# Kernel optimization log

Hardware: AMD Instinct MI355X
Metric: run time of the kernel (lower is better)

## Reference

```python
import jax, jax.numpy as jnp
import numpy as np

B, T, C = 4, 1024, 1024
H, D = 16, 64  # num_heads, head_channels
EPS = 1e-5


def layernorm(x, g, b):
    mu = jnp.mean(x, axis=-1, keepdims=True)
    d = x - mu
    var = jnp.mean(d * d, axis=-1, keepdims=True)
    return d * jax.lax.rsqrt(var + EPS) * g + b


def setup_inputs() -> dict:
    key = jax.random.key(0)
    ks = jax.random.split(key, 5)
    s = 0.02  # init scale for weights
    return {
        "x": jax.random.normal(ks[0], (B, T, C), jnp.float32),
        "norm_g": jnp.ones((C,), jnp.float32),
        "norm_b": jnp.zeros((C,), jnp.float32),
        "qkv_w": jax.random.normal(ks[1], (C, 3 * C), jnp.float32) * s,
        "qkv_b": jax.random.normal(ks[2], (3 * C,), jnp.float32) * s,
        "qln_g": jnp.ones((C,), jnp.float32),
        "qln_b": jnp.zeros((C,), jnp.float32),
        "kln_g": jnp.ones((C,), jnp.float32),
        "kln_b": jnp.zeros((C,), jnp.float32),
        "proj_w": jax.random.normal(ks[3], (C, C), jnp.float32) * s,
        "proj_b": jax.random.normal(ks[4], (C,), jnp.float32) * s,
    }


def reference(x, norm_g, norm_b, qkv_w, qkv_b, qln_g, qln_b, kln_g, kln_b, proj_w, proj_b):
    in_dtype = x.dtype
    # pre-LN computed in fp32, cast back to input dtype
    xn = layernorm(x.astype(jnp.float32), norm_g, norm_b).astype(in_dtype)
    qkv = xn @ qkv_w + qkv_b  # [B,T,3C]
    q, k, v = jnp.split(qkv, 3, axis=-1)
    # per-Q/K LayerNorm over the full channel dim (before head split)
    q = layernorm(q, qln_g, qln_b)
    k = layernorm(k, kln_g, kln_b)
    # [B,T,C] -> [B,H,T,D]
    to_heads = lambda t: t.reshape(B, T, H, D).transpose(0, 2, 1, 3)
    q, k, v = to_heads(q), to_heads(k), to_heads(v)
    temp = 1.0
    scale = (D ** -0.5) / temp  # sqrt_scale**2 / temp
    scores = jnp.einsum("bhqd,bhkd->bhqk", q, k) * scale
    attn = jax.nn.softmax(scores, axis=-1)
    out = jnp.einsum("bhqk,bhkd->bhqd", attn, v)
    out = out.transpose(0, 2, 1, 3).reshape(B, T, C)
    return out @ proj_w + proj_b
```

## Files before the change

kernel.cpp:

```cpp
#include <hip/hip_runtime.h>
#include <math.h>

#define T_SEQ 1024
#define C_DIM 1024
#define NB    4
#define NH    16
#define HD    64
#define C3    3072

typedef __attribute__((ext_vector_type(8))) short bf16x8;
typedef __attribute__((ext_vector_type(4))) float f32x4;
typedef unsigned short u16;

union B8 { bf16x8 v; u16 u[8]; unsigned d[4]; };

__device__ inline u16 bf16_rtn(float v) {
    unsigned int u = __float_as_uint(v);
    u += 0x7FFFu + ((u >> 16) & 1u);
    return (u16)(u >> 16);
}
__device__ inline void split_bf16(float v, u16& hi, u16& lo) {
    hi = bf16_rtn(v);
    float hif = __uint_as_float(((unsigned int)hi) << 16);
    lo = bf16_rtn(v - hif);
}

__global__ __launch_bounds__(256) void ln_split_kernel(const float* __restrict__ in,
                                                       u16* __restrict__ oh,
                                                       u16* __restrict__ ol,
                                                       const float* __restrict__ g,
                                                       const float* __restrict__ beta) {
    const int row = blockIdx.x;
    const float* x = in + (size_t)row * 1024;
    const int t = threadIdx.x;

    float4 v = *(const float4*)&x[t * 4];
    float s  = v.x + v.y + v.z + v.w;
    float ss = v.x * v.x + v.y * v.y + v.z * v.z + v.w * v.w;
    #pragma unroll
    for (int m = 1; m < 64; m <<= 1) {
        s  += __shfl_xor(s, m);
        ss += __shfl_xor(ss, m);
    }
    __shared__ float red[8];
    const int wave = t >> 6, lane = t & 63;
    if (lane == 0) { red[wave * 2] = s; red[wave * 2 + 1] = ss; }
    __syncthreads();
    s  = red[0] + red[2] + red[4] + red[6];
    ss = red[1] + red[3] + red[5] + red[7];

    const float mu   = s * (1.0f / 1024.0f);
    const float var  = ss * (1.0f / 1024.0f) - mu * mu;
    const float rstd = rsqrtf(var + 1e-5f);

    float4 gg = *(const float4*)&g[t * 4];
    float4 bb = *(const float4*)&beta[t * 4];
    float o[4];
    o[0] = (v.x - mu) * rstd * gg.x + bb.x;
    o[1] = (v.y - mu) * rstd * gg.y + bb.y;
    o[2] = (v.z - mu) * rstd * gg.z + bb.z;
    o[3] = (v.w - mu) * rstd * gg.w + bb.w;

    ushort4 h4, l4;
    split_bf16(o[0], h4.x, l4.x);
    split_bf16(o[1], h4.y, l4.y);
    split_bf16(o[2], h4.z, l4.z);
    split_bf16(o[3], h4.w, l4.w);
    size_t off = (size_t)row * 1024 + t * 4;
    *(ushort4*)&oh[off] = h4;
    *(ushort4*)&ol[off] = l4;
}

__global__ __launch_bounds__(256) void ln_qk_kernel(float* __restrict__ qkv,
                                                    const float* __restrict__ qg,
                                                    const float* __restrict__ qb,
                                                    const float* __restrict__ kg,
                                                    const float* __restrict__ kb,
                                                    u16* __restrict__ Kh,
                                                    u16* __restrict__ Kl) {
    const int row = blockIdx.x;
    const int isK = row >> 12;
    const int r = row & 4095;
    float* x = qkv + (size_t)r * C3 + (isK ? 1024 : 0);
    const float* g    = isK ? kg : qg;
    const float* beta = isK ? kb : qb;
    const int t = threadIdx.x;

    float4 v = *(const float4*)&x[t * 4];
    float s  = v.x + v.y + v.z + v.w;
    float ss = v.x * v.x + v.y * v.y + v.z * v.z + v.w * v.w;
    #pragma unroll
    for (int m = 1; m < 64; m <<= 1) {
        s  += __shfl_xor(s, m);
        ss += __shfl_xor(ss, m);
    }
    __shared__ float red[8];
    const int wave = t >> 6, lane = t & 63;
    if (lane == 0) { red[wave * 2] = s; red[wave * 2 + 1] = ss; }
    __syncthreads();
    s  = red[0] + red[2] + red[4] + red[6];
    ss = red[1] + red[3] + red[5] + red[7];

    const float mu   = s * (1.0f / 1024.0f);
    const float var  = ss * (1.0f / 1024.0f) - mu * mu;
    const float rstd = rsqrtf(var + 1e-5f);

    float4 gg = *(const float4*)&g[t * 4];
    float4 bb = *(const float4*)&beta[t * 4];
    float o0 = (v.x - mu) * rstd * gg.x + bb.x;
    float o1 = (v.y - mu) * rstd * gg.y + bb.y;
    float o2 = (v.z - mu) * rstd * gg.z + bb.z;
    float o3 = (v.w - mu) * rstd * gg.w + bb.w;

    if (!isK) {
        float4 o = {o0, o1, o2, o3};
        *(float4*)&x[t * 4] = o;
    } else {
        ushort4 h4, l4;
        split_bf16(o0, h4.x, l4.x);
        split_bf16(o1, h4.y, l4.y);
        split_bf16(o2, h4.z, l4.z);
        split_bf16(o3, h4.w, l4.w);
        const int c = t * 4;
        const int hh = c >> 6, d = c & 63;
        const int b = r >> 10, tt = r & 1023;
        size_t off = ((size_t)((b << 4) + hh) << 16) + (size_t)tt * 64 + d;
        *(ushort4*)&Kh[off] = h4;
        *(ushort4*)&Kl[off] = l4;
    }
}

__global__ __launch_bounds__(256) void vsplit_t(const float* __restrict__ qkv,
                                                u16* __restrict__ Vth,
                                                u16* __restrict__ Vtl) {
    __shared__ float tile[64][68];
    const int bid = blockIdx.x;
    const int tt = bid & 15, h = (bid >> 4) & 15, b = bid >> 8;
    const int t = threadIdx.x;
    const float* src = qkv + (size_t)(b * 1024 + tt * 64) * C3 + 2048 + h * 64;
    #pragma unroll
    for (int i = 0; i < 4; ++i) {
        int idx = i * 256 + t;
        int tr = idx >> 4, dc = (idx & 15) * 4;
        float4 v = *(const float4*)&src[(size_t)tr * C3 + dc];
        tile[tr][dc + 0] = v.x; tile[tr][dc + 1] = v.y;
        tile[tr][dc + 2] = v.z; tile[tr][dc + 3] = v.w;
    }
    __syncthreads();
    #pragma unroll
    for (int i = 0; i < 4; ++i) {
        int idx = i * 256 + t;
        int d = idx >> 4, tc = (idx & 15) * 4;
        ushort4 h4, l4;
        split_bf16(tile[tc + 0][d], h4.x, l4.x);
        split_bf16(tile[tc + 1][d], h4.y, l4.y);
        split_bf16(tile[tc + 2][d], h4.z, l4.z);
        split_bf16(tile[tc + 3][d], h4.w, l4.w);
        size_t off = ((size_t)((b * 16 + h) * 64 + d)) * 1024 + tt * 64 + tc;
        *(ushort4*)&Vth[off] = h4;
        *(ushort4*)&Vtl[off] = l4;
    }
}

__global__ __launch_bounds__(256) void wsplit_t(const float* __restrict__ W,
                                                u16* __restrict__ Th,
                                                u16* __restrict__ Tl,
                                                int K, int N, int ldt) {
    __shared__ float tile[64][69];
    const int n0 = blockIdx.x * 64, k0 = blockIdx.y * 64;
    const int t = threadIdx.x;
    #pragma unroll
    for (int i = 0; i < 4; ++i) {
        int idx = t + 256 * i;
        int kr = idx >> 4, nc = (idx & 15) * 4;
        float4 v = *(const float4*)&W[(size_t)(k0 + kr) * N + n0 + nc];
        tile[kr][nc + 0] = v.x; tile[kr][nc + 1] = v.y;
        tile[kr][nc + 2] = v.z; tile[kr][nc + 3] = v.w;
    }
    __syncthreads();
    #pragma unroll
    for (int i = 0; i < 4; ++i) {
        int idx = t + 256 * i;
        int nr = idx >> 4, kc = (idx & 15) * 4;
        ushort4 h4, l4;
        split_bf16(tile[kc + 0][nr], h4.x, l4.x);
        split_bf16(tile[kc + 1][nr], h4.y, l4.y);
        split_bf16(tile[kc + 2][nr], h4.z, l4.z);
        split_bf16(tile[kc + 3][nr], h4.w, l4.w);
        size_t o = (size_t)(n0 + nr) * ldt + k0 + kc;
        *(ushort4*)&Th[o] = h4;
        *(ushort4*)&Tl[o] = l4;
    }
}

__global__ __launch_bounds__(512, 2) void gemm256_mfma_split(
    const u16* __restrict__ Ah, const u16* __restrict__ Al,
    const u16* __restrict__ Bh, const u16* __restrict__ Bl,
    const float* __restrict__ bias, float* __restrict__ C,
    int N, int lda, int ldb) {
    __shared__ __align__(16) u16 SM[65536];

    const int t    = threadIdx.x;
    const int lane = t & 63;
    const int wid  = t >> 6;
    const int wr   = wid >> 2;
    const int wc   = wid & 3;
    const int m16  = lane & 15, g8 = lane >> 4;

    const int nbx = gridDim.x;
    const int nwg = nbx * gridDim.y;
    int bid = blockIdx.y * nbx + blockIdx.x;
    int swz = (bid & 7) * (nwg >> 3) + (bid >> 3);
    const int bn = (swz % nbx) * 256;
    const int bm = (swz / nbx) * 256;

    f32x4 acc[8][4];
    #pragma unroll
    for (int m = 0; m < 8; ++m)
        #pragma unroll
        for (int n = 0; n < 4; ++n) {
            f32x4 z = {0.0f, 0.0f, 0.0f, 0.0f};
            acc[m][n] = z;
        }

    auto STAGE = [&](int tile, int buf) {
        const int reg = tile >> 4;
        const u16* Ab = (reg == 1) ? Al : Ah;
        const u16* Bb = (reg == 2) ? Bl : Bh;
        const int kloc = (tile & 15) << 6;
        #pragma unroll
        for (int i = 0; i < 4; ++i) {
            const int idx = i * 512 + t;
            const int r = idx >> 3;
            const int cl = (idx & 7) ^ (r & 7);
            const size_t ga = ((size_t)(bm + r) * lda + kloc + cl * 8) * 2;
            const size_t gb = ((size_t)(bn + r) * ldb + kloc + cl * 8) * 2;
            const unsigned la = (unsigned)(buf * 32768 + idx * 16);
            const unsigned lb = (unsigned)(65536 + buf * 32768 + idx * 16);
            __builtin_amdgcn_global_load_lds(
                (const __attribute__((address_space(1))) void*)((const char*)Ab + ga),
                (__attribute__((address_space(3))) void*)((char*)SM + la), 16, 0, 0);
            __builtin_amdgcn_global_load_lds(
                (const __attribute__((address_space(1))) void*)((const char*)Bb + gb),
                (__attribute__((address_space(3))) void*)((char*)SM + lb), 16, 0, 0);
        }
    };

    STAGE(0, 0);
    STAGE(1, 1);
    asm volatile("s_waitcnt vmcnt(8)" ::: "memory");
    __builtin_amdgcn_s_barrier();
    __builtin_amdgcn_sched_barrier(0);

    for (int tt = 0; tt < 48; ++tt) {
        const int cb = tt & 1;
        const u16* Abuf = SM + cb * 16384;
        const u16* Bbuf = SM + 32768 + cb * 16384;

        bf16x8 bf[4][2];
        #pragma unroll
        for (int n = 0; n < 4; ++n)
            #pragma unroll
            for (int ks = 0; ks < 2; ++ks) {
                const int r = wc * 64 + n * 16 + m16;
                bf[n][ks] = *(const bf16x8*)&Bbuf[r * 64 + (((ks * 4 + g8) ^ (r & 7)) << 3)];
            }
        __builtin_amdgcn_s_setprio(1);
        #pragma unroll
        for (int m = 0; m < 8; ++m) {
            const int r = wr * 128 + m * 16 + m16;
            bf16x8 a0 = *(const bf16x8*)&Abuf[r * 64 + ((g8 ^ (r & 7)) << 3)];
            bf16x8 a1 = *(const bf16x8*)&Abuf[r * 64 + (((4 + g8) ^ (r & 7)) << 3)];
            #pragma unroll
            for (int n = 0; n < 4; ++n) {
                acc[m][n] = __builtin_amdgcn_mfma_f32_16x16x32_bf16(a0, bf[n][0], acc[m][n], 0, 0, 0);
                acc[m][n] = __builtin_amdgcn_mfma_f32_16x16x32_bf16(a1, bf[n][1], acc[m][n], 0, 0, 0);
            }
        }
        __builtin_amdgcn_s_setprio(0);

        __builtin_amdgcn_sched_barrier(0);
        __builtin_amdgcn_s_barrier();
        __builtin_amdgcn_sched_barrier(0);
        if (tt + 2 < 48) {
            STAGE(tt + 2, cb);
            __builtin_amdgcn_sched_barrier(0);
            asm volatile("s_waitcnt vmcnt(8)" ::: "memory");
        } else {
            asm volatile("s_waitcnt vmcnt(0)" ::: "memory");
        }
        __builtin_amdgcn_sched_barrier(0);
        __builtin_amdgcn_s_barrier();
        __builtin_amdgcn_sched_barrier(0);
    }

    #pragma unroll
    for (int m = 0; m < 8; ++m) {
        const int row0 = bm + wr * 128 + m * 16 + (g8 << 2);
        #pragma unroll
        for (int n = 0; n < 4; ++n) {
            const int col = bn + wc * 64 + n * 16 + m16;
            const float bv = bias[col];
            #pragma unroll
            for (int e = 0; e < 4; ++e)
                C[(size_t)(row0 + e) * N + col] = acc[m][n][e] + bv;
        }
    }
}

__global__ __launch_bounds__(256) void gemm_mfma_split(
    const u16* __restrict__ Ah, const u16* __restrict__ Al,
    const u16* __restrict__ Bh, const u16* __restrict__ Bl,
    const float* __restrict__ bias, float* __restrict__ C,
    int M, int N, int K, int lda, int ldb) {
    __shared__ u16 sAh[128 * 32], sAl[128 * 32], sBh[128 * 32], sBl[128 * 32];

    const int t    = threadIdx.x;
    const int lane = t & 63;
    const int wid  = t >> 6;
    const int wr   = wid >> 1, wc = wid & 1;

    const int nbx = gridDim.x;
    const int nwg = nbx * gridDim.y;
    int bid = blockIdx.y * nbx + blockIdx.x;
    int swz = (bid & 7) * (nwg >> 3) + (bid >> 3);
    const int bn = (swz % nbx) * 128;
    const int bm = (swz / nbx) * 128;

    const int jr    = lane >> 2;
    const int cphys = lane & 3;
    const int m16 = lane & 15, g8 = lane >> 4;

    f32x4 acc[4][4];
    #pragma unroll
    for (int m = 0; m < 4; ++m)
        #pragma unroll
        for (int n = 0; n < 4; ++n) {
            f32x4 z = {0.0f, 0.0f, 0.0f, 0.0f};
            acc[m][n] = z;
        }

    for (int k0 = 0; k0 < K; k0 += 32) {
        __syncthreads();
        #pragma unroll
        for (int jj = 0; jj < 2; ++jj) {
            const int j = wid * 2 + jj;
            const int r = (j << 4) + jr;
            const int cl = cphys ^ (r & 3);
            const size_t ga = ((size_t)(bm + r) * lda + k0 + (cl << 3)) * 2;
            const size_t gb = ((size_t)(bn + r) * ldb + k0 + (cl << 3)) * 2;
            const unsigned ldso = (unsigned)(j << 10);
            __builtin_amdgcn_global_load_lds(
                (const __attribute__((address_space(1))) void*)((const char*)Ah + ga),
                (__attribute__((address_space(3))) void*)((char*)sAh + ldso), 16, 0, 0);
            __builtin_amdgcn_global_load_lds(
                (const __attribute__((address_space(1))) void*)((const char*)Al + ga),
                (__attribute__((address_space(3))) void*)((char*)sAl + ldso), 16, 0, 0);
            __builtin_amdgcn_global_load_lds(
                (const __attribute__((address_space(1))) void*)((const char*)Bh + gb),
                (__attribute__((address_space(3))) void*)((char*)sBh + ldso), 16, 0, 0);
            __builtin_amdgcn_global_load_lds(
                (const __attribute__((address_space(1))) void*)((const char*)Bl + gb),
                (__attribute__((address_space(3))) void*)((char*)sBl + ldso), 16, 0, 0);
        }
        __syncthreads();

        bf16x8 ah[4], al[4], bh[4], bl[4];
        #pragma unroll
        for (int m = 0; m < 4; ++m) {
            const int r = wr * 64 + m * 16 + m16;
            const int off = (r << 5) + ((g8 ^ (m16 & 3)) << 3);
            ah[m] = *(const bf16x8*)&sAh[off];
            al[m] = *(const bf16x8*)&sAl[off];
        }
        #pragma unroll
        for (int n = 0; n < 4; ++n) {
            const int r = wc * 64 + n * 16 + m16;
            const int off = (r << 5) + ((g8 ^ (m16 & 3)) << 3);
            bh[n] = *(const bf16x8*)&sBh[off];
            bl[n] = *(const bf16x8*)&sBl[off];
        }
        #pragma unroll
        for (int m = 0; m < 4; ++m)
            #pragma unroll
            for (int n = 0; n < 4; ++n) {
                acc[m][n] = __builtin_amdgcn_mfma_f32_16x16x32_bf16(ah[m], bh[n], acc[m][n], 0, 0, 0);
                acc[m][n] = __builtin_amdgcn_mfma_f32_16x16x32_bf16(al[m], bh[n], acc[m][n], 0, 0, 0);
                acc[m][n] = __builtin_amdgcn_mfma_f32_16x16x32_bf16(ah[m], bl[n], acc[m][n], 0, 0, 0);
            }
    }

    #pragma unroll
    for (int m = 0; m < 4; ++m) {
        const int row0 = bm + wr * 64 + m * 16 + (g8 << 2);
        #pragma unroll
        for (int n = 0; n < 4; ++n) {
            const int col = bn + wc * 64 + n * 16 + m16;
            const float bv = bias[col];
            #pragma unroll
            for (int e = 0; e < 4; ++e)
                C[(size_t)(row0 + e) * N + col] = acc[m][n][e] + bv;
        }
    }
}

__global__ __launch_bounds__(256) void attn_mfma(const float* __restrict__ qkv,
                                                 const u16* __restrict__ Kh,
                                                 const u16* __restrict__ Kl,
                                                 const u16* __restrict__ Vth,
                                                 const u16* __restrict__ Vtl,
                                                 u16* __restrict__ att) {
    __shared__ __align__(16) u16 SM[32768];

    const int t    = threadIdx.x;
    const int lane = t & 63;
    const int wv   = t >> 6;
    const int m16  = lane & 15, g8 = lane >> 4;

    const int bid  = blockIdx.x;
    const int work = (bid & 7) * 128 + (bid >> 3);
    const int qt = work & 15;
    const int bh = work >> 4;
    const int h  = bh & 15;
    const int b  = bh >> 4;
    const int q0 = qt * 64;

    const int srow = lane >> 3;
    const int scl  = (lane & 7) ^ srow;
    const size_t kvrow0 = (size_t)bh << 16;

    auto stageK = [&](int kt) {
        const int kb = kt * 64;
        #pragma unroll
        for (int issue = 0; issue < 2; ++issue) {
            const int rloc = (issue * 4 + wv) * 8 + srow;
            const size_t go = (kvrow0 + (size_t)(kb + rloc) * 64 + scl * 8) * 2;
            const unsigned lo = (unsigned)((issue * 4 + wv) * 1024);
            __builtin_amdgcn_global_load_lds(
                (const __attribute__((address_space(1))) void*)((const char*)Kh + go),
                (__attribute__((address_space(3))) void*)((char*)SM + lo), 16, 0, 0);
            __builtin_amdgcn_global_load_lds(
                (const __attribute__((address_space(1))) void*)((const char*)Kl + go),
                (__attribute__((address_space(3))) void*)((char*)SM + 8192 + lo), 16, 0, 0);
        }
    };
    auto stageV = [&](int kt, int bsel) {
        const int kb = kt * 64;
        #pragma unroll
        for (int issue = 0; issue < 2; ++issue) {
            const int rloc = (issue * 4 + wv) * 8 + srow;
            const size_t go = (kvrow0 + (size_t)rloc * 1024 + kb + scl * 8) * 2;
            const unsigned lo = (unsigned)(16384 + bsel * 16384 + (issue * 4 + wv) * 1024);
            __builtin_amdgcn_global_load_lds(
                (const __attribute__((address_space(1))) void*)((const char*)Vth + go),
                (__attribute__((address_space(3))) void*)((char*)SM + lo), 16, 0, 0);
            __builtin_amdgcn_global_load_lds(
                (const __attribute__((address_space(1))) void*)((const char*)Vtl + go),
                (__attribute__((address_space(3))) void*)((char*)SM + 8192 + lo), 16, 0, 0);
        }
    };

    bf16x8 qh[2], ql[2];
    {
        const float* qrow = qkv + (size_t)(b * T_SEQ + q0 + wv * 16 + m16) * C3 + h * HD;
        #pragma unroll
        for (int ds = 0; ds < 2; ++ds) {
            float4 a = *(const float4*)&qrow[ds * 32 + g8 * 8];
            float4 c = *(const float4*)&qrow[ds * 32 + g8 * 8 + 4];
            float q8[8] = {a.x, a.y, a.z, a.w, c.x, c.y, c.z, c.w};
            B8 hh, ll;
            #pragma unroll
            for (int j = 0; j < 8; ++j) {
                u16 hi, lo;
                split_bf16(q8[j] * 0.125f, hi, lo);
                hh.u[j] = hi; ll.u[j] = lo;
            }
            qh[ds] = hh.v; ql[ds] = ll.v;
        }
    }

    f32x4 acc_o[4];
    #pragma unroll
    for (int i = 0; i < 4; ++i) { f32x4 z = {0, 0, 0, 0}; acc_o[i] = z; }
    float m_run = -INFINITY, l_run = 0.0f;

    u16* Phw = SM + 24576 + wv * 1024;
    u16* Plw = SM + 28672 + wv * 1024;

    stageK(0);
    stageV(0, 0);
    asm volatile("s_waitcnt vmcnt(0)" ::: "memory");
    __builtin_amdgcn_s_barrier();
    __builtin_amdgcn_sched_barrier(0);

    int vsel = 0;
    for (int kt = 0; kt < 16; ++kt) {
        f32x4 accs[4];
        #pragma unroll
        for (int i = 0; i < 4; ++i) { f32x4 z = {0, 0, 0, 0}; accs[i] = z; }
        #pragma unroll
        for (int ds = 0; ds < 2; ++ds) {
            #pragma unroll
            for (int sub = 0; sub < 4; ++sub) {
                const int row = sub * 16 + m16;
                const int idx = row * 64 + ((((ds * 4 + g8)) ^ (m16 & 7)) << 3);
                bf16x8 kh = *(const bf16x8*)&SM[idx];
                bf16x8 kl = *(const bf16x8*)&SM[4096 + idx];
                accs[sub] = __builtin_amdgcn_mfma_f32_16x16x32_bf16(kh, qh[ds], accs[sub], 0, 0, 0);
                accs[sub] = __builtin_amdgcn_mfma_f32_16x16x32_bf16(kl, qh[ds], accs[sub], 0, 0, 0);
                accs[sub] = __builtin_amdgcn_mfma_f32_16x16x32_bf16(kh, ql[ds], accs[sub], 0, 0, 0);
            }
        }

        __builtin_amdgcn_sched_barrier(0);
        __builtin_amdgcn_s_barrier();
        __builtin_amdgcn_sched_barrier(0);
        if (kt < 15) { stageK(kt + 1); stageV(kt + 1, vsel ^ 1); }

        float mt = accs[0][0];
        #pragma unroll
        for (int sub = 0; sub < 4; ++sub)
            #pragma unroll
            for (int e = 0; e < 4; ++e) mt = fmaxf(mt, accs[sub][e]);
        mt = fmaxf(mt, __shfl_xor(mt, 16));
        mt = fmaxf(mt, __shfl_xor(mt, 32));
        const float mnew = fmaxf(m_run, mt);
        const float fsc = __expf(m_run - mnew);
        float p[4][4];
        float ts = 0.0f;
        #pragma unroll
        for (int sub = 0; sub < 4; ++sub)
            #pragma unroll
            for (int e = 0; e < 4; ++e) {
                p[sub][e] = __expf(accs[sub][e] - mnew);
                ts += p[sub][e];
            }
        ts += __shfl_xor(ts, 16);
        ts += __shfl_xor(ts, 32);
        l_run = l_run * fsc + ts;
        m_run = mnew;
        #pragma unroll
        for (int d = 0; d < 4; ++d)
            #pragma unroll
            for (int e = 0; e < 4; ++e) acc_o[d][e] *= fsc;

        #pragma unroll
        for (int sub = 0; sub < 4; ++sub)
            #pragma unroll
            for (int pp = 0; pp < 2; ++pp) {
                float p0 = p[sub][2 * pp], p1 = p[sub][2 * pp + 1];
                u16 h0, l0, h1, l1;
                split_bf16(p0, h0, l0);
                split_bf16(p1, h1, l1);
                unsigned hw = (unsigned)h0 | ((unsigned)h1 << 16);
                unsigned lw = (unsigned)l0 | ((unsigned)l1 << 16);
                const int idx = m16 * 64 + (((2 * sub + (g8 >> 1)) ^ (m16 & 7)) << 3)
                                + 4 * (g8 & 1) + 2 * pp;
                *(unsigned*)&Phw[idx] = hw;
                *(unsigned*)&Plw[idx] = lw;
            }

        bf16x8 pfh[2], pfl[2];
        #pragma unroll
        for (int ks = 0; ks < 2; ++ks) {
            const int idx = m16 * 64 + ((((ks * 4 + g8)) ^ (m16 & 7)) << 3);
            pfh[ks] = *(const bf16x8*)&Phw[idx];
            pfl[ks] = *(const bf16x8*)&Plw[idx];
        }

        const int vb = 8192 + vsel * 8192;
        #pragma unroll
        for (int dsub = 0; dsub < 4; ++dsub) {
            #pragma unroll
            for (int ks = 0; ks < 2; ++ks) {
                const int vrow = dsub * 16 + m16;
                const int vidx = vb + vrow * 64 + ((((ks * 4 + g8)) ^ (m16 & 7)) << 3);
                bf16x8 vh = *(const bf16x8*)&SM[vidx];
                bf16x8 vl = *(const bf16x8*)&SM[4096 + vidx];
                acc_o[dsub] = __builtin_amdgcn_mfma_f32_16x16x32_bf16(vh, pfh[ks], acc_o[dsub], 0, 0, 0);
                acc_o[dsub] = __builtin_amdgcn_mfma_f32_16x16x32_bf16(vh, pfl[ks], acc_o[dsub], 0, 0, 0);
                acc_o[dsub] = __builtin_amdgcn_mfma_f32_16x16x32_bf16(vl, pfh[ks], acc_o[dsub], 0, 0, 0);
            }
        }

        __builtin_amdgcn_sched_barrier(0);
        asm volatile("s_waitcnt vmcnt(0)" ::: "memory");
        __builtin_amdgcn_s_barrier();
        __builtin_amdgcn_sched_barrier(0);
        vsel ^= 1;
    }

    const float linv = 1.0f / l_run;
    #pragma unroll
    for (int dsub = 0; dsub < 4; ++dsub)
        #pragma unroll
        for (int pp = 0; pp < 2; ++pp) {
            float o0 = acc_o[dsub][2 * pp] * linv;
            float o1 = acc_o[dsub][2 * pp + 1] * linv;
            u16 h0, l0, h1, l1;
            split_bf16(o0, h0, l0);
            split_bf16(o1, h1, l1);
            unsigned hw = (unsigned)h0 | ((unsigned)h1 << 16);
            unsigned lw = (unsigned)l0 | ((unsigned)l1 << 16);
            const int idx = m16 * 64 + (((2 * dsub + (g8 >> 1)) ^ (m16 & 7)) << 3)
                            + 4 * (g8 & 1) + 2 * pp;
            *(unsigned*)&Phw[idx] = hw;
            *(unsigned*)&Plw[idx] = lw;
        }
    __syncthreads();
    #pragma unroll
    for (int i = 0; i < 2; ++i) {
        int s = t + 256 * i;
        int q_l = s >> 3, dg8 = s & 7;
        const int idx = q_l * 64 + ((dg8 ^ (q_l & 7)) << 3);
        bf16x8 oh = *(const bf16x8*)&SM[24576 + idx];
        bf16x8 ol = *(const bf16x8*)&SM[28672 + idx];
        size_t off = (size_t)(b * T_SEQ + q0 + q_l) * 6144 + 2048 + h * HD + dg8 * 8;
        *(bf16x8*)&att[off] = oh;
        *(bf16x8*)&att[off + 1024] = ol;
    }
}

extern "C" void kernel_launch(void* const* d_in, const int* in_sizes, int n_in,
                              void* d_out, int out_size, void* d_ws, size_t ws_size,
                              hipStream_t stream) {
    const float* x      = (const float*)d_in[0];
    const float* norm_g = (const float*)d_in[1];
    const float* norm_b = (const float*)d_in[2];
    const float* qkv_w  = (const float*)d_in[3];
    const float* qkv_b  = (const float*)d_in[4];
    const float* qln_g  = (const float*)d_in[5];
    const float* qln_b  = (const float*)d_in[6];
    const float* kln_g  = (const float*)d_in[7];
    const float* kln_b  = (const float*)d_in[8];
    const float* proj_w = (const float*)d_in[9];
    const float* proj_b = (const float*)d_in[10];
    float* out = (float*)d_out;

    char* w = (char*)d_ws;
    float* qkv    = (float*)w;
    u16* qkv_u16  = (u16*)w;
    u16* xn_hi    = (u16*)(w + 50331648);
    u16* xn_lo    = (u16*)(w + 58720256);
    u16* wq_hi    = (u16*)(w + 67108864);
    u16* wq_lo    = (u16*)(w + 73400320);
    u16* Kh       = xn_hi;
    u16* Kl       = xn_lo;
    u16* Vth      = (u16*)(w + 67108864);
    u16* Vtl      = (u16*)(w + 75497472);
    u16* pw_hi    = qkv_u16 + 4096;
    u16* pw_lo    = qkv_u16 + 5120;
    u16* att_hi   = qkv_u16 + 2048;
    u16* att_lo   = qkv_u16 + 3072;

    const int rows = NB * T_SEQ;

    ln_split_kernel<<<rows, 256, 0, stream>>>(x, xn_hi, xn_lo, norm_g, norm_b);
    wsplit_t<<<dim3(C3 / 64, C_DIM / 64), 256, 0, stream>>>(qkv_w, wq_hi, wq_lo, C_DIM, C3, 1024);
    gemm256_mfma_split<<<dim3(C3 / 256, rows / 256), 512, 0, stream>>>(
        xn_hi, xn_lo, wq_hi, wq_lo, qkv_b, qkv, C3, 1024, 1024);
    ln_qk_kernel<<<2 * rows, 256, 0, stream>>>(qkv, qln_g, qln_b, kln_g, kln_b, Kh, Kl);
    vsplit_t<<<1024, 256, 0, stream>>>(qkv, Vth, Vtl);
    wsplit_t<<<dim3(C_DIM / 64, C_DIM / 64), 256, 0, stream>>>(proj_w, pw_hi, pw_lo, C_DIM, C_DIM, 6144);
    attn_mfma<<<1024, 256, 0, stream>>>(qkv, Kh, Kl, Vth, Vtl, qkv_u16);
    gemm_mfma_split<<<dim3(C_DIM / 128, rows / 128), 256, 0, stream>>>(
        att_hi, att_lo, pw_hi, pw_lo, proj_b, out, rows, C_DIM, C_DIM, 6144, 6144);
}
```

Measured before the change: 330.5 us.

## Restructure QKV GEMM mainloop into four-phase interleaved load/compute pipeline

Rewrites the 256x256 split-bf16 QKV GEMM main loop so each K-tile is split into two 32-wide halves stored in separate LDS regions. Global-to-LDS staging is issued in small per-wave chunks interleaved with four MFMA phases per iteration, with barriers between phases. The goal is to overlap memory traffic with MFMA work more finely and cut register pressure from the fragment loads. Launch bounds drop from 2 to 1 waves per SIMD, which allows more registers but may lower occupancy. The extra barriers and the more intricate vmcnt accounting add synchronization cost and room for ordering errors.

```diff
diff --git a/kernel.cpp b/kernel.cpp
--- a/kernel.cpp
+++ b/kernel.cpp
@@ -193,7 +193,7 @@
     }
 }
 
-__global__ __launch_bounds__(512, 2) void gemm256_mfma_split(
+__global__ __launch_bounds__(512, 1) void gemm256_8ph(
     const u16* __restrict__ Ah, const u16* __restrict__ Al,
     const u16* __restrict__ Bh, const u16* __restrict__ Bl,
     const float* __restrict__ bias, float* __restrict__ C,
@@ -223,71 +223,130 @@
             acc[m][n] = z;
         }
 
-    auto STAGE = [&](int tile, int buf) {
+    const int srow = lane >> 2;
+    const int scol = lane & 3;
+
+    auto STAGE1 = [&](int tile, int ks, int part, int buf) {
+        if (tile > 47) return;
         const int reg = tile >> 4;
-        const u16* Ab = (reg == 1) ? Al : Ah;
-        const u16* Bb = (reg == 2) ? Bl : Bh;
-        const int kloc = (tile & 15) << 6;
-        #pragma unroll
-        for (int i = 0; i < 4; ++i) {
-            const int idx = i * 512 + t;
-            const int r = idx >> 3;
-            const int cl = (idx & 7) ^ (r & 7);
-            const size_t ga = ((size_t)(bm + r) * lda + kloc + cl * 8) * 2;
-            const size_t gb = ((size_t)(bn + r) * ldb + kloc + cl * 8) * 2;
-            const unsigned la = (unsigned)(buf * 32768 + idx * 16);
-            const unsigned lb = (unsigned)(65536 + buf * 32768 + idx * 16);
-            __builtin_amdgcn_global_load_lds(
-                (const __attribute__((address_space(1))) void*)((const char*)Ab + ga),
-                (__attribute__((address_space(3))) void*)((char*)SM + la), 16, 0, 0);
-            __builtin_amdgcn_global_load_lds(
-                (const __attribute__((address_space(1))) void*)((const char*)Bb + gb),
-                (__attribute__((address_space(3))) void*)((char*)SM + lb), 16, 0, 0);
+        const u16* src = part == 0 ? ((reg == 1) ? Al : Ah)
+                                   : ((reg == 2) ? Bl : Bh);
+        const int ld = part == 0 ? lda : ldb;
+        const int r0 = part == 0 ? bm : bn;
+        const int kloc = ((tile & 15) << 6) + (ks << 5);
+        const unsigned mb = (unsigned)(part * 65536 + buf * 32768 + ks * 16384 + wid * 2048);
+        #pragma unroll
+        for (int j = 0; j < 2; ++j) {
+            const int row = wid * 32 + j * 16 + srow;
+            const int cl = scol ^ (row & 3);
+            const size_t ga = ((size_t)(r0 + row) * ld + kloc + cl * 8) * 2;
+            __builtin_amdgcn_global_load_lds(
+                (const __attribute__((address_space(1))) void*)((const char*)src + ga),
+                (__attribute__((address_space(3))) void*)((char*)SM + mb + j * 1024),
+                16, 0, 0);
         }
     };
 
-    STAGE(0, 0);
-    STAGE(1, 1);
+    STAGE1(0, 0, 0, 0); STAGE1(0, 0, 1, 0);
+    STAGE1(0, 1, 0, 0); STAGE1(0, 1, 1, 0);
+    STAGE1(1, 0, 0, 1); STAGE1(1, 0, 1, 1);
+    __builtin_amdgcn_sched_barrier(0);
     asm volatile("s_waitcnt vmcnt(8)" ::: "memory");
+    __builtin_amdgcn_sched_barrier(0);
     __builtin_amdgcn_s_barrier();
     __builtin_amdgcn_sched_barrier(0);
 
     for (int tt = 0; tt < 48; ++tt) {
         const int cb = tt & 1;
-        const u16* Abuf = SM + cb * 16384;
-        const u16* Bbuf = SM + 32768 + cb * 16384;
-
-        bf16x8 bf[4][2];
-        #pragma unroll
-        for (int n = 0; n < 4; ++n)
-            #pragma unroll
-            for (int ks = 0; ks < 2; ++ks) {
-                const int r = wc * 64 + n * 16 + m16;
-                bf[n][ks] = *(const bf16x8*)&Bbuf[r * 64 + (((ks * 4 + g8) ^ (r & 7)) << 3)];
-            }
+        const int aB = cb * 16384;
+        const int bB = 32768 + cb * 16384;
+        bf16x8 bfr[4], afr[4];
+
+        #pragma unroll
+        for (int n = 0; n < 4; ++n) {
+            const int r = wc * 64 + n * 16 + m16;
+            bfr[n] = *(const bf16x8*)&SM[bB + r * 32 + ((g8 ^ (r & 3)) << 3)];
+        }
+        #pragma unroll
+        for (int m = 0; m < 4; ++m) {
+            const int r = wr * 128 + m * 16 + m16;
+            afr[m] = *(const bf16x8*)&SM[aB + r * 32 + ((g8 ^ (r & 3)) << 3)];
+        }
+        STAGE1(tt + 1, 1, 0, cb ^ 1);
         __builtin_amdgcn_s_setprio(1);
         #pragma unroll
-        for (int m = 0; m < 8; ++m) {
-            const int r = wr * 128 + m * 16 + m16;
-            bf16x8 a0 = *(const bf16x8*)&Abuf[r * 64 + ((g8 ^ (r & 7)) << 3)];
-            bf16x8 a1 = *(const bf16x8*)&Abuf[r * 64 + (((4 + g8) ^ (r & 7)) << 3)];
-            #pragma unroll
-            for (int n = 0; n < 4; ++n) {
-                acc[m][n] = __builtin_amdgcn_mfma_f32_16x16x32_bf16(a0, bf[n][0], acc[m][n], 0, 0, 0);
-                acc[m][n] = __builtin_amdgcn_mfma_f32_16x16x32_bf16(a1, bf[n][1], acc[m][n], 0, 0, 0);
-            }
-        }
+        for (int m = 0; m < 4; ++m)
+            #pragma unroll
+            for (int n = 0; n < 4; ++n)
+                acc[m][n] = __builtin_amdgcn_mfma_f32_16x16x32_bf16(afr[m], bfr[n], acc[m][n], 0, 0, 0);
         __builtin_amdgcn_s_setprio(0);
-
         __builtin_amdgcn_sched_barrier(0);
         __builtin_amdgcn_s_barrier();
         __builtin_amdgcn_sched_barrier(0);
-        if (tt + 2 < 48) {
-            STAGE(tt + 2, cb);
-            __builtin_amdgcn_sched_barrier(0);
+
+        #pragma unroll
+        for (int m = 0; m < 4; ++m) {
+            const int r = wr * 128 + (m + 4) * 16 + m16;
+            afr[m] = *(const bf16x8*)&SM[aB + r * 32 + ((g8 ^ (r & 3)) << 3)];
+        }
+        STAGE1(tt + 1, 1, 1, cb ^ 1);
+        __builtin_amdgcn_s_setprio(1);
+        #pragma unroll
+        for (int m = 0; m < 4; ++m)
+            #pragma unroll
+            for (int n = 0; n < 4; ++n)
+                acc[m + 4][n] = __builtin_amdgcn_mfma_f32_16x16x32_bf16(afr[m], bfr[n], acc[m + 4][n], 0, 0, 0);
+        __builtin_amdgcn_s_setprio(0);
+        __builtin_amdgcn_sched_barrier(0);
+        if (tt < 47) {
             asm volatile("s_waitcnt vmcnt(8)" ::: "memory");
         } else {
             asm volatile("s_waitcnt vmcnt(0)" ::: "memory");
+        }
+        __builtin_amdgcn_sched_barrier(0);
+        __builtin_amdgcn_s_barrier();
+        __builtin_amdgcn_sched_barrier(0);
+
+        #pragma unroll
+        for (int n = 0; n < 4; ++n) {
+            const int r = wc * 64 + n * 16 + m16;
+            bfr[n] = *(const bf16x8*)&SM[bB + 8192 + r * 32 + ((g8 ^ (r & 3)) << 3)];
+        }
+        #pragma unroll
+        for (int m = 0; m < 4; ++m) {
+            const int r = wr * 128 + m * 16 + m16;
+            afr[m] = *(const bf16x8*)&SM[aB + 8192 + r * 32 + ((g8 ^ (r & 3)) << 3)];
+        }
+        STAGE1(tt + 2, 0, 0, cb);
+        __builtin_amdgcn_s_setprio(1);
+        #pragma unroll
+        for (int m = 0; m < 4; ++m)
+            #pragma unroll
+            for (int n = 0; n < 4; ++n)
+                acc[m][n] = __builtin_amdgcn_mfma_f32_16x16x32_bf16(afr[m], bfr[n], acc[m][n], 0, 0, 0);
+        __builtin_amdgcn_s_setprio(0);
+        __builtin_amdgcn_sched_barrier(0);
+        __builtin_amdgcn_s_barrier();
+        __builtin_amdgcn_sched_barrier(0);
+
+        #pragma unroll
+        for (int m = 0; m < 4; ++m) {
+            const int r = wr * 128 + (m + 4) * 16 + m16;
+            afr[m] = *(const bf16x8*)&SM[aB + 8192 + r * 32 + ((g8 ^ (r & 3)) << 3)];
+        }
+        STAGE1(tt + 2, 0, 1, cb);
+        __builtin_amdgcn_s_setprio(1);
+        #pragma unroll
+        for (int m = 0; m < 4; ++m)
+            #pragma unroll
+            for (int n = 0; n < 4; ++n)
+                acc[m + 4][n] = __builtin_amdgcn_mfma_f32_16x16x32_bf16(afr[m], bfr[n], acc[m + 4][n], 0, 0, 0);
+        __builtin_amdgcn_s_setprio(0);
+        __builtin_amdgcn_sched_barrier(0);
+        if (tt < 46) {
+            asm volatile("s_waitcnt vmcnt(8)" ::: "memory");
+        } else if (tt == 46) {
+            asm volatile("s_waitcnt vmcnt(4)" ::: "memory");
         }
         __builtin_amdgcn_sched_barrier(0);
         __builtin_amdgcn_s_barrier();
@@ -657,7 +716,7 @@
 
     ln_split_kernel<<<rows, 256, 0, stream>>>(x, xn_hi, xn_lo, norm_g, norm_b);
     wsplit_t<<<dim3(C3 / 64, C_DIM / 64), 256, 0, stream>>>(qkv_w, wq_hi, wq_lo, C_DIM, C3, 1024);
-    gemm256_mfma_split<<<dim3(C3 / 256, rows / 256), 512, 0, stream>>>(
+    gemm256_8ph<<<dim3(C3 / 256, rows / 256), 512, 0, stream>>>(
         xn_hi, xn_lo, wq_hi, wq_lo, qkv_b, qkv, C3, 1024, 1024);
     ln_qk_kernel<<<2 * rows, 256, 0, stream>>>(qkv, qln_g, qln_b, kln_g, kln_b, Kh, Kl);
     vsplit_t<<<1024, 256, 0, stream>>>(qkv, Vth, Vtl);
```

Result: no change. 330.6 us (+0.0%).
